# Kernel tuning notes

Hardware: AMD Instinct MI355X
Metric: run time of the kernel (lower is better)

## Reference

```python
import jax, jax.numpy as jnp
import numpy as np

STEPS = 3


def setup_inputs() -> dict:
    key = jax.random.key(0)
    ks = jax.random.split(key, 6)
    N, H, B = 1000000, 128, 16384
    x = jax.random.normal(ks[0], (N, H), dtype=jnp.float32)
    batch_vec = jnp.sort(jax.random.randint(ks[1], (N,), 0, B)).astype(jnp.int64)
    scale_ih = 1.0 / np.sqrt(2 * H)
    scale_hh = 1.0 / np.sqrt(H)
    W_ih = jax.random.normal(ks[2], (4 * H, 2 * H), dtype=jnp.float32) * scale_ih
    W_hh = jax.random.normal(ks[3], (4 * H, H), dtype=jnp.float32) * scale_hh
    b_ih = jnp.zeros((4 * H,), dtype=jnp.float32)
    b_hh = jnp.zeros((4 * H,), dtype=jnp.float32)
    return {"x": x, "batch_vec": batch_vec, "W_ih": W_ih, "W_hh": W_hh,
            "b_ih": b_ih, "b_hh": b_hh, "num_graphs": B}


def _set2set(x, batch_vec, W_ih, W_hh, b_ih, b_hh, B):
    N, H = x.shape
    q_star = jnp.zeros((B, 2 * H), x.dtype)
    h = jnp.zeros((B, H), x.dtype)
    c = jnp.zeros((B, H), x.dtype)
    bias = b_ih + b_hh
    for _ in range(STEPS):
        # LSTMCell (torch gate order: i, f, g, o)
        gates = q_star @ W_ih.T + h @ W_hh.T + bias  # [B, 4H]
        i, f, g, o = jnp.split(gates, 4, axis=-1)
        c = jax.nn.sigmoid(f) * c + jax.nn.sigmoid(i) * jnp.tanh(g)
        h = jax.nn.sigmoid(o) * jnp.tanh(c)
        q = h  # [B, H]
        # attention logits per node
        e = jnp.sum(x * q[batch_vec], axis=-1)  # [N]
        emax = jax.ops.segment_max(e, batch_vec, num_segments=B)
        emax = jax.lax.stop_gradient(jnp.where(jnp.isfinite(emax), emax, 0.0))
        ex = jnp.exp(e - emax[batch_vec])
        denom = jax.ops.segment_sum(ex, batch_vec, num_segments=B)
        a = ex / denom[batch_vec]  # segment softmax, [N]
        r = jax.ops.segment_sum(a[:, None] * x, batch_vec, num_segments=B)  # [B, H]
        q_star = jnp.concatenate([q, r], axis=-1)  # [B, 2H]
    return q_star


def reference(x, batch_vec, W_ih, W_hh, b_ih, b_hh, num_graphs):
    return _set2set(x, batch_vec, W_ih, W_hh, b_ih, b_hh, int(num_graphs))
```

## Files before the change

### kernel.cpp

```cpp
#include <hip/hip_runtime.h>
#include <math.h>

#define HDIM 128
#define G4 512
#define TS 36

typedef float vf4 __attribute__((ext_vector_type(4)));
typedef unsigned short u16x8 __attribute__((ext_vector_type(8)));

__device__ __forceinline__ float sigm(float v) { return 1.0f / (1.0f + __expf(-v)); }
__device__ __forceinline__ float ftanh(float v) {
    return 1.0f - 2.0f / (__expf(2.0f * v) + 1.0f);
}
__device__ __forceinline__ float dot4(vf4 a, vf4 b) {
    return a.x * b.x + a.y * b.y + a.z * b.z + a.w * b.w;
}
__device__ __forceinline__ vf4 ldnt4(const float* p) {
    return __builtin_nontemporal_load((const vf4*)p);
}
__device__ __forceinline__ unsigned short f2bf(float f) {
    unsigned u = __float_as_uint(f);
    u += 0x7fff + ((u >> 16) & 1);
    return (unsigned short)(u >> 16);
}
__device__ __forceinline__ float bf2f(unsigned short h) {
    return __uint_as_float(((unsigned)h) << 16);
}

__global__ __launch_bounds__(256) void k_setup(const float* __restrict__ W_ih,
                                               const float* __restrict__ W_hh,
                                               const float* __restrict__ b_ih,
                                               const float* __restrict__ b_hh,
                                               const int* __restrict__ batch_vec, int N, int B,
                                               float* __restrict__ Wc, int* __restrict__ seg_start,
                                               float* __restrict__ gh0) {
    __shared__ float h0s[HDIM];
    int t = blockIdx.x * 256 + threadIdx.x;
    if (blockIdx.x < 2) {
        if (threadIdx.x < HDIM) {
            int hid = threadIdx.x;
            float bi = b_ih[hid] + b_hh[hid];
            float bg = b_ih[2 * HDIM + hid] + b_hh[2 * HDIM + hid];
            float bo = b_ih[3 * HDIM + hid] + b_hh[3 * HDIM + hid];
            float c0 = sigm(bi) * ftanh(bg);
            h0s[hid] = sigm(bo) * ftanh(c0);
        }
        __syncthreads();
        if (t < G4) {
            float s = 0.0f;
#pragma unroll
            for (int k = 0; k < HDIM; k += 4) {
                vf4 wi = *(const vf4*)(W_ih + (size_t)t * 256 + k);
                vf4 wh = *(const vf4*)(W_hh + (size_t)t * HDIM + k);
                s += (wi.x + wh.x) * h0s[k] + (wi.y + wh.y) * h0s[k + 1] +
                     (wi.z + wh.z) * h0s[k + 2] + (wi.w + wh.w) * h0s[k + 3];
            }
            gh0[t] = s;
        }
    }
    if (t < G4 * 2 * HDIM) {
        int g = t >> 8;
        int k = t & 255;
        float w = W_ih[g * 256 + k];
        if (k < HDIM) w += W_hh[g * HDIM + k];
        Wc[t] = w;
    }
    if (t <= B) {
        int lo = 0, hi = N;
        while (lo < hi) {
            int mid = (lo + hi) >> 1;
            if (batch_vec[mid] < t) lo = mid + 1; else hi = mid;
        }
        seg_start[t] = lo;
    }
}

__global__ __launch_bounds__(256) void k_cvt(const float* __restrict__ x,
                                             unsigned short* __restrict__ x16,
                                             long total8) {
    long i = (long)blockIdx.x * 256 + threadIdx.x;
    long stride = (long)gridDim.x * 256;
    for (; i < total8; i += stride) {
        vf4 a = ldnt4(x + i * 8);
        vf4 b = ldnt4(x + i * 8 + 4);
        u16x8 c;
        c[0] = f2bf(a.x); c[1] = f2bf(a.y); c[2] = f2bf(a.z); c[3] = f2bf(a.w);
        c[4] = f2bf(b.x); c[5] = f2bf(b.y); c[6] = f2bf(b.z); c[7] = f2bf(b.w);
        *(u16x8*)(x16 + i * 8) = c;
    }
}

#define UPD(m_, d_, ra_, rb_, p_, xa_, xb_)  \
    {                                        \
        float mn_ = fmaxf(m_, p_);           \
        float sc_ = __expf(m_ - mn_);        \
        float pe_ = __expf(p_ - mn_);        \
        d_ = d_ * sc_ + pe_;                 \
        ra_ = ra_ * sc_ + pe_ * xa_;         \
        rb_ = rb_ * sc_ + pe_ * xb_;         \
        m_ = mn_;                            \
    }

#define SHFL16(p_)                  \
    p_ += __shfl_xor(p_, 1, 64);    \
    p_ += __shfl_xor(p_, 2, 64);    \
    p_ += __shfl_xor(p_, 4, 64);    \
    p_ += __shfl_xor(p_, 8, 64);

__global__ __launch_bounds__(256) void k_attn(const unsigned short* __restrict__ x16,
                                              const float* __restrict__ q, int ldq,
                                              const float* __restrict__ b_ih,
                                              const float* __restrict__ b_hh,
                                              const int* __restrict__ seg_start,
                                              float* __restrict__ r_out, int ldr, int col_off,
                                              int B) {
    int wave = threadIdx.x >> 6;
    int lane = threadIdx.x & 63;
    int l16 = lane & 15;
    int quarter = lane >> 4;
    int nblk = gridDim.x;
    int bid = blockIdx.x;
    int q8 = nblk >> 3, r8 = nblk & 7;
    int xcd = bid & 7, pos = bid >> 3;
    int nb = (xcd < r8 ? xcd * (q8 + 1) : r8 * (q8 + 1) + (xcd - r8) * q8) + pos;
    int seg = (nb << 2) + wave;
    if (seg >= B) return;
    int s = seg_start[seg], e = seg_start[seg + 1];

    vf4 qa, qb;
    if (q) {
        const float* qrow = q + (size_t)seg * ldq + l16 * 8;
        qa = *(const vf4*)qrow;
        qb = *(const vf4*)(qrow + 4);
    } else {
        int c = l16 * 8;
        vf4 bi0 = *(const vf4*)(b_ih + c) + *(const vf4*)(b_hh + c);
        vf4 bi1 = *(const vf4*)(b_ih + c + 4) + *(const vf4*)(b_hh + c + 4);
        vf4 bg0 = *(const vf4*)(b_ih + 2 * HDIM + c) + *(const vf4*)(b_hh + 2 * HDIM + c);
        vf4 bg1 = *(const vf4*)(b_ih + 2 * HDIM + c + 4) + *(const vf4*)(b_hh + 2 * HDIM + c + 4);
        vf4 bo0 = *(const vf4*)(b_ih + 3 * HDIM + c) + *(const vf4*)(b_hh + 3 * HDIM + c);
        vf4 bo1 = *(const vf4*)(b_ih + 3 * HDIM + c + 4) + *(const vf4*)(b_hh + 3 * HDIM + c + 4);
#pragma unroll
        for (int j = 0; j < 4; ++j) {
            float c0 = sigm(bi0[j]) * ftanh(bg0[j]);
            qa[j] = sigm(bo0[j]) * ftanh(c0);
            float c1 = sigm(bi1[j]) * ftanh(bg1[j]);
            qb[j] = sigm(bo1[j]) * ftanh(c1);
        }
    }

    float m0 = 0.0f, d0 = 0.0f, m1 = 0.0f, d1 = 0.0f;
    vf4 ra0 = {0.f, 0.f, 0.f, 0.f}, rb0 = {0.f, 0.f, 0.f, 0.f};
    vf4 ra1 = {0.f, 0.f, 0.f, 0.f}, rb1 = {0.f, 0.f, 0.f, 0.f};

    int base = s;
#pragma unroll 1
    for (; base + 16 <= e; base += 16) {
        vf4 xa[4], xb[4];
        float p[4];
#pragma unroll
        for (int t = 0; t < 4; ++t) {
            const unsigned short* xr = x16 + (size_t)(base + quarter + 4 * t) * HDIM + l16 * 8;
            u16x8 u = *(const u16x8*)xr;
            xa[t] = vf4{bf2f(u[0]), bf2f(u[1]), bf2f(u[2]), bf2f(u[3])};
            xb[t] = vf4{bf2f(u[4]), bf2f(u[5]), bf2f(u[6]), bf2f(u[7])};
        }
#pragma unroll
        for (int t = 0; t < 4; ++t) p[t] = dot4(xa[t], qa) + dot4(xb[t], qb);
        SHFL16(p[0]) SHFL16(p[1]) SHFL16(p[2]) SHFL16(p[3])
        UPD(m0, d0, ra0, rb0, p[0], xa[0], xb[0])
        UPD(m1, d1, ra1, rb1, p[1], xa[1], xb[1])
        UPD(m0, d0, ra0, rb0, p[2], xa[2], xb[2])
        UPD(m1, d1, ra1, rb1, p[3], xa[3], xb[3])
    }
#pragma unroll 1
    for (; base < e; base += 4) {
        int row = base + quarter;
        const unsigned short* xr = x16 + (size_t)min(row, e - 1) * HDIM + l16 * 8;
        u16x8 u = *(const u16x8*)xr;
        vf4 xa = {bf2f(u[0]), bf2f(u[1]), bf2f(u[2]), bf2f(u[3])};
        vf4 xb = {bf2f(u[4]), bf2f(u[5]), bf2f(u[6]), bf2f(u[7])};
        float p = dot4(xa, qa) + dot4(xb, qb);
        SHFL16(p)
        if (row >= e) p = -1e30f;
        UPD(m0, d0, ra0, rb0, p, xa, xb)
    }
    {
        float M = fmaxf(m0, m1);
        float w0 = __expf(m0 - M), w1 = __expf(m1 - M);
        d0 = d0 * w0 + d1 * w1;
        ra0 = ra0 * w0 + ra1 * w1;
        rb0 = rb0 * w0 + rb1 * w1;
        m0 = M;
    }
#pragma unroll
    for (int off = 16; off <= 32; off <<= 1) {
        float om = __shfl_xor(m0, off, 64);
        float M = fmaxf(m0, om);
        float w = __expf(m0 - M);
        d0 *= w; ra0 *= w; rb0 *= w;
        d0 += __shfl_xor(d0, off, 64);
        ra0.x += __shfl_xor(ra0.x, off, 64);
        ra0.y += __shfl_xor(ra0.y, off, 64);
        ra0.z += __shfl_xor(ra0.z, off, 64);
        ra0.w += __shfl_xor(ra0.w, off, 64);
        rb0.x += __shfl_xor(rb0.x, off, 64);
        rb0.y += __shfl_xor(rb0.y, off, 64);
        rb0.z += __shfl_xor(rb0.z, off, 64);
        rb0.w += __shfl_xor(rb0.w, off, 64);
        m0 = M;
    }
    float inv = (d0 > 0.0f) ? 1.0f / d0 : 0.0f;
    if (quarter == 0) {
        float* dst = r_out + (size_t)seg * ldr + col_off + l16 * 8;
        *(vf4*)dst = ra0 * inv;
        *(vf4*)(dst + 4) = rb0 * inv;
    }
}

__global__ __launch_bounds__(256) void k_gemm_lstm1(const float* __restrict__ r_prev,
                                                    const float* __restrict__ Wc,
                                                    const float* __restrict__ gh0,
                                                    const float* __restrict__ b_ih,
                                                    const float* __restrict__ b_hh,
                                                    float* __restrict__ h_new,
                                                    float* __restrict__ c_new) {
    __shared__ float As[128 * TS];
    __shared__ float Ws[64 * TS];
    int ct = blockIdx.y;
    int rb = blockIdx.x * 128;
    int tid = threadIdx.x;
    int tx = tid & 15, ty = tid >> 4;
    float acc[8][4];
#pragma unroll
    for (int i = 0; i < 8; ++i)
#pragma unroll
        for (int j = 0; j < 4; ++j) acc[i][j] = 0.0f;

    for (int kc = 0; kc < 4; ++kc) {
        int kbase = kc * 32;
#pragma unroll
        for (int i = 0; i < 4; ++i) {
            int li = tid + i * 256;
            int row = li >> 3;
            int c4 = (li & 7) * 4;
            *(vf4*)&As[row * TS + c4] = *(const vf4*)(r_prev + (size_t)(rb + row) * HDIM + kbase + c4);
        }
#pragma unroll
        for (int i = 0; i < 2; ++i) {
            int li = tid + i * 256;
            int col = li >> 3;
            int c4 = (li & 7) * 4;
            int g = ct * 16 + (col & 15) + 128 * (col >> 4);
            *(vf4*)&Ws[col * TS + c4] = *(const vf4*)(Wc + (size_t)g * 256 + 128 + kbase + c4);
        }
        __syncthreads();
#pragma unroll
        for (int k = 0; k < 32; k += 4) {
            vf4 a[8], b[4];
#pragma unroll
            for (int i = 0; i < 8; ++i) a[i] = *(vf4*)&As[(ty + 16 * i) * TS + k];
#pragma unroll
            for (int j = 0; j < 4; ++j) b[j] = *(vf4*)&Ws[(tx + 16 * j) * TS + k];
#pragma unroll
            for (int i = 0; i < 8; ++i)
#pragma unroll
                for (int j = 0; j < 4; ++j) {
                    acc[i][j] += a[i].x * b[j].x + a[i].y * b[j].y +
                                 a[i].z * b[j].z + a[i].w * b[j].w;
                }
        }
        __syncthreads();
    }
    int hidx = ct * 16 + tx;
    float bi = b_ih[hidx] + b_hh[hidx] + gh0[hidx];
    float bf = b_ih[HDIM + hidx] + b_hh[HDIM + hidx] + gh0[HDIM + hidx];
    float bg = b_ih[2 * HDIM + hidx] + b_hh[2 * HDIM + hidx] + gh0[2 * HDIM + hidx];
    float bo = b_ih[3 * HDIM + hidx] + b_hh[3 * HDIM + hidx] + gh0[3 * HDIM + hidx];
    float bi0 = b_ih[hidx] + b_hh[hidx];
    float bg0 = b_ih[2 * HDIM + hidx] + b_hh[2 * HDIM + hidx];
    float c0 = sigm(bi0) * ftanh(bg0);
#pragma unroll
    for (int i = 0; i < 8; ++i) {
        int row = rb + ty + 16 * i;
        float gi = acc[i][0] + bi;
        float gf = acc[i][1] + bf;
        float gg = acc[i][2] + bg;
        float go = acc[i][3] + bo;
        float cn = sigm(gf) * c0 + sigm(gi) * ftanh(gg);
        float hn = sigm(go) * ftanh(cn);
        c_new[(size_t)row * HDIM + hidx] = cn;
        h_new[(size_t)row * HDIM + hidx] = hn;
    }
}

__global__ __launch_bounds__(256) void k_gemm_lstm(const float* __restrict__ h_prev,
                                                   const float* __restrict__ r_prev,
                                                   const float* __restrict__ c_prev,
                                                   const float* __restrict__ Wc,
                                                   const float* __restrict__ b_ih,
                                                   const float* __restrict__ b_hh,
                                                   float* __restrict__ h_mirror) {
    __shared__ float As[128 * TS];
    __shared__ float Ws[64 * TS];
    int ct = blockIdx.y;
    int rb = blockIdx.x * 128;
    int tid = threadIdx.x;
    int tx = tid & 15, ty = tid >> 4;
    float acc[8][4];
#pragma unroll
    for (int i = 0; i < 8; ++i)
#pragma unroll
        for (int j = 0; j < 4; ++j) acc[i][j] = 0.0f;

    for (int kc = 0; kc < 8; ++kc) {
        const float* src = (kc < 4) ? h_prev : r_prev;
        int kbase = (kc & 3) * 32;
#pragma unroll
        for (int i = 0; i < 4; ++i) {
            int li = tid + i * 256;
            int row = li >> 3;
            int c4 = (li & 7) * 4;
            *(vf4*)&As[row * TS + c4] = *(const vf4*)(src + (size_t)(rb + row) * HDIM + kbase + c4);
        }
#pragma unroll
        for (int i = 0; i < 2; ++i) {
            int li = tid + i * 256;
            int col = li >> 3;
            int c4 = (li & 7) * 4;
            int g = ct * 16 + (col & 15) + 128 * (col >> 4);
            *(vf4*)&Ws[col * TS + c4] = *(const vf4*)(Wc + (size_t)g * 256 + kc * 32 + c4);
        }
        __syncthreads();
#pragma unroll
        for (int k = 0; k < 32; k += 4) {
            vf4 a[8], b[4];
#pragma unroll
            for (int i = 0; i < 8; ++i) a[i] = *(vf4*)&As[(ty + 16 * i) * TS + k];
#pragma unroll
            for (int j = 0; j < 4; ++j) b[j] = *(vf4*)&Ws[(tx + 16 * j) * TS + k];
#pragma unroll
            for (int i = 0; i < 8; ++i)
#pragma unroll
                for (int j = 0; j < 4; ++j) {
                    acc[i][j] += a[i].x * b[j].x + a[i].y * b[j].y +
                                 a[i].z * b[j].z + a[i].w * b[j].w;
                }
        }
        __syncthreads();
    }
    int hidx = ct * 16 + tx;
    float bi = b_ih[hidx] + b_hh[hidx];
    float bf = b_ih[HDIM + hidx] + b_hh[HDIM + hidx];
    float bg = b_ih[2 * HDIM + hidx] + b_hh[2 * HDIM + hidx];
    float bo = b_ih[3 * HDIM + hidx] + b_hh[3 * HDIM + hidx];
#pragma unroll
    for (int i = 0; i < 8; ++i) {
        int row = rb + ty + 16 * i;
        float gi = acc[i][0] + bi;
        float gf = acc[i][1] + bf;
        float gg = acc[i][2] + bg;
        float go = acc[i][3] + bo;
        float cp = c_prev[(size_t)row * HDIM + hidx];
        float cn = sigm(gf) * cp + sigm(gi) * ftanh(gg);
        float hn = sigm(go) * ftanh(cn);
        h_mirror[(size_t)row * 2 * HDIM + hidx] = hn;
    }
}

extern "C" void kernel_launch(void* const* d_in, const int* in_sizes, int n_in,
                              void* d_out, int out_size, void* d_ws, size_t ws_size,
                              hipStream_t stream) {
    const float* x = (const float*)d_in[0];
    const int* batch_vec = (const int*)d_in[1];
    const float* W_ih = (const float*)d_in[2];
    const float* W_hh = (const float*)d_in[3];
    const float* b_ih = (const float*)d_in[4];
    const float* b_hh = (const float*)d_in[5];
    float* out = (float*)d_out;

    int N = in_sizes[1];
    int B = out_size / (2 * HDIM);

    char* ws = (char*)d_ws;
    float* Wc = (float*)ws;            ws += (size_t)G4 * 2 * HDIM * 4;
    float* gh0 = (float*)ws;           ws += (size_t)G4 * 4;
    float* h_b = (float*)ws;           ws += (size_t)B * HDIM * 4;
    float* cbuf = (float*)ws;          ws += (size_t)B * HDIM * 4;
    float* rbuf = (float*)ws;          ws += (size_t)B * HDIM * 4;
    int* seg = (int*)ws;               ws += (size_t)(B + 1) * 4;
    ws = (char*)(((size_t)ws + 255) & ~(size_t)255);
    unsigned short* x16 = (unsigned short*)ws;

    k_setup<<<512, 256, 0, stream>>>(W_ih, W_hh, b_ih, b_hh, batch_vec, N, B, Wc, seg, gh0);
    k_cvt<<<2048, 256, 0, stream>>>(x, x16, (long)N * HDIM / 8);

    dim3 ggrid(B / 128, 8);
    int ablk = (B + 3) / 4;
    k_attn<<<ablk, 256, 0, stream>>>(x16, nullptr, 0, b_ih, b_hh, seg, rbuf, HDIM, 0, B);
    k_gemm_lstm1<<<ggrid, 256, 0, stream>>>(rbuf, Wc, gh0, b_ih, b_hh, h_b, cbuf);
    k_attn<<<ablk, 256, 0, stream>>>(x16, h_b, HDIM, b_ih, b_hh, seg, rbuf, HDIM, 0, B);
    k_gemm_lstm<<<ggrid, 256, 0, stream>>>(h_b, rbuf, cbuf, Wc, b_ih, b_hh, out);
    k_attn<<<ablk, 256, 0, stream>>>(x16, out, 2 * HDIM, b_ih, b_hh, seg, out, 2 * HDIM, HDIM, B);
}
```

Baseline: 476.7 us.

## Fuse bf16 conversion into first attention pass and give each 16-lane group one segment

Drops the separate fp32-to-bf16 conversion kernel. The first attention pass now reads fp32 x directly, converts it, and writes x16 while computing the step-0 attention. This removes one full extra read of x. All attention passes now map one segment to each 16-lane quarter instead of one per wave, with software-prefetched rows and no cross-quarter reduction, and the middle pass walks blocks in reverse order to reuse cached x16 data. The risks are load imbalance inside a wave when segment lengths differ, since every quarter loops to the longest segment, plus higher register pressure from the prefetch buffers.

```diff
diff --git a/kernel.cpp b/kernel.cpp
--- a/kernel.cpp
+++ b/kernel.cpp
@@ -75,21 +75,6 @@
     }
 }
 
-__global__ __launch_bounds__(256) void k_cvt(const float* __restrict__ x,
-                                             unsigned short* __restrict__ x16,
-                                             long total8) {
-    long i = (long)blockIdx.x * 256 + threadIdx.x;
-    long stride = (long)gridDim.x * 256;
-    for (; i < total8; i += stride) {
-        vf4 a = ldnt4(x + i * 8);
-        vf4 b = ldnt4(x + i * 8 + 4);
-        u16x8 c;
-        c[0] = f2bf(a.x); c[1] = f2bf(a.y); c[2] = f2bf(a.z); c[3] = f2bf(a.w);
-        c[4] = f2bf(b.x); c[5] = f2bf(b.y); c[6] = f2bf(b.z); c[7] = f2bf(b.w);
-        *(u16x8*)(x16 + i * 8) = c;
-    }
-}
-
 #define UPD(m_, d_, ra_, rb_, p_, xa_, xb_)  \
     {                                        \
         float mn_ = fmaxf(m_, p_);           \
@@ -107,32 +92,68 @@
     p_ += __shfl_xor(p_, 4, 64);    \
     p_ += __shfl_xor(p_, 8, 64);
 
-__global__ __launch_bounds__(256) void k_attn(const unsigned short* __restrict__ x16,
-                                              const float* __restrict__ q, int ldq,
-                                              const float* __restrict__ b_ih,
-                                              const float* __restrict__ b_hh,
-                                              const int* __restrict__ seg_start,
-                                              float* __restrict__ r_out, int ldr, int col_off,
-                                              int B) {
+struct AttState {
+    float m0, d0, m1, d1;
+    vf4 ra0, rb0, ra1, rb1;
+};
+
+__device__ __forceinline__ void init_state(AttState& st) {
+    st.m0 = 0.f; st.d0 = 0.f; st.m1 = 0.f; st.d1 = 0.f;
+    st.ra0 = vf4{0.f, 0.f, 0.f, 0.f}; st.rb0 = vf4{0.f, 0.f, 0.f, 0.f};
+    st.ra1 = vf4{0.f, 0.f, 0.f, 0.f}; st.rb1 = vf4{0.f, 0.f, 0.f, 0.f};
+}
+
+__device__ __forceinline__ void compute4(const vf4 xa[4], const vf4 xb[4], int baserow, int e,
+                                         vf4 qa, vf4 qb, AttState& st) {
+    float p[4];
+#pragma unroll
+    for (int t = 0; t < 4; ++t) p[t] = dot4(xa[t], qa) + dot4(xb[t], qb);
+    SHFL16(p[0]) SHFL16(p[1]) SHFL16(p[2]) SHFL16(p[3])
+#pragma unroll
+    for (int t = 0; t < 4; ++t)
+        if (baserow + t >= e) p[t] = -1e30f;
+    UPD(st.m0, st.d0, st.ra0, st.rb0, p[0], xa[0], xb[0])
+    UPD(st.m1, st.d1, st.ra1, st.rb1, p[1], xa[1], xb[1])
+    UPD(st.m0, st.d0, st.ra0, st.rb0, p[2], xa[2], xb[2])
+    UPD(st.m1, st.d1, st.ra1, st.rb1, p[3], xa[3], xb[3])
+}
+
+__device__ __forceinline__ void finish_state(AttState& st, float* dst) {
+    float M = fmaxf(st.m0, st.m1);
+    float w0 = __expf(st.m0 - M), w1 = __expf(st.m1 - M);
+    float d = st.d0 * w0 + st.d1 * w1;
+    vf4 ra = st.ra0 * w0 + st.ra1 * w1;
+    vf4 rb = st.rb0 * w0 + st.rb1 * w1;
+    float inv = (d > 0.0f) ? 1.0f / d : 0.0f;
+    *(vf4*)dst = ra * inv;
+    *(vf4*)(dst + 4) = rb * inv;
+}
+
+__device__ __forceinline__ int seg_of_block(int bid, int nblk, int rev, int wave, int quarter) {
+    int q8 = nblk >> 3, r8 = nblk & 7;
+    int xcd = bid & 7, pos = bid >> 3;
+    int nb = (xcd < r8 ? xcd * (q8 + 1) : r8 * (q8 + 1) + (xcd - r8) * q8) + pos;
+    if (rev) nb = nblk - 1 - nb;
+    return nb * 16 + wave * 4 + quarter;
+}
+
+__global__ __launch_bounds__(256) void k_attn_cvt(const float* __restrict__ x,
+                                                  unsigned short* __restrict__ x16,
+                                                  const float* __restrict__ b_ih,
+                                                  const float* __restrict__ b_hh,
+                                                  const int* __restrict__ seg_start,
+                                                  float* __restrict__ r_out, int B) {
     int wave = threadIdx.x >> 6;
     int lane = threadIdx.x & 63;
     int l16 = lane & 15;
     int quarter = lane >> 4;
-    int nblk = gridDim.x;
-    int bid = blockIdx.x;
-    int q8 = nblk >> 3, r8 = nblk & 7;
-    int xcd = bid & 7, pos = bid >> 3;
-    int nb = (xcd < r8 ? xcd * (q8 + 1) : r8 * (q8 + 1) + (xcd - r8) * q8) + pos;
-    int seg = (nb << 2) + wave;
-    if (seg >= B) return;
-    int s = seg_start[seg], e = seg_start[seg + 1];
+    int seg = seg_of_block(blockIdx.x, gridDim.x, 0, wave, quarter);
+    int seg_c = min(seg, B - 1);
+    int s = seg_start[seg_c], e = seg_start[seg_c + 1];
+    if (seg >= B) { s = 0; e = 0; }
 
     vf4 qa, qb;
-    if (q) {
-        const float* qrow = q + (size_t)seg * ldq + l16 * 8;
-        qa = *(const vf4*)qrow;
-        qb = *(const vf4*)(qrow + 4);
-    } else {
+    {
         int c = l16 * 8;
         vf4 bi0 = *(const vf4*)(b_ih + c) + *(const vf4*)(b_hh + c);
         vf4 bi1 = *(const vf4*)(b_ih + c + 4) + *(const vf4*)(b_hh + c + 4);
@@ -149,73 +170,124 @@
         }
     }
 
-    float m0 = 0.0f, d0 = 0.0f, m1 = 0.0f, d1 = 0.0f;
-    vf4 ra0 = {0.f, 0.f, 0.f, 0.f}, rb0 = {0.f, 0.f, 0.f, 0.f};
-    vf4 ra1 = {0.f, 0.f, 0.f, 0.f}, rb1 = {0.f, 0.f, 0.f, 0.f};
-
+    int iters = (e - s + 3) >> 2;
+    iters = max(iters, __shfl_xor(iters, 16, 64));
+    iters = max(iters, __shfl_xor(iters, 32, 64));
+    iters = max(iters, 1);
+
+    AttState st;
+    init_state(st);
+
+    vf4 ca[4], cb[4];
+#pragma unroll
+    for (int t = 0; t < 4; ++t) {
+        int rl = max(min(s + t, e - 1), 0);
+        const float* xr = x + (size_t)rl * HDIM + l16 * 8;
+        ca[t] = ldnt4(xr);
+        cb[t] = ldnt4(xr + 4);
+    }
     int base = s;
 #pragma unroll 1
-    for (; base + 16 <= e; base += 16) {
+    for (int j = 1; j < iters; ++j) {
+        vf4 na[4], nb[4];
+#pragma unroll
+        for (int t = 0; t < 4; ++t) {
+            int rl = max(min(s + 4 * j + t, e - 1), 0);
+            const float* xr = x + (size_t)rl * HDIM + l16 * 8;
+            na[t] = ldnt4(xr);
+            nb[t] = ldnt4(xr + 4);
+        }
+#pragma unroll
+        for (int t = 0; t < 4; ++t) {
+            if (base + t < e) {
+                u16x8 cv;
+                cv[0] = f2bf(ca[t].x); cv[1] = f2bf(ca[t].y); cv[2] = f2bf(ca[t].z); cv[3] = f2bf(ca[t].w);
+                cv[4] = f2bf(cb[t].x); cv[5] = f2bf(cb[t].y); cv[6] = f2bf(cb[t].z); cv[7] = f2bf(cb[t].w);
+                *(u16x8*)(x16 + (size_t)(base + t) * HDIM + l16 * 8) = cv;
+            }
+        }
+        compute4(ca, cb, base, e, qa, qb, st);
+#pragma unroll
+        for (int t = 0; t < 4; ++t) { ca[t] = na[t]; cb[t] = nb[t]; }
+        base += 4;
+    }
+#pragma unroll
+    for (int t = 0; t < 4; ++t) {
+        if (base + t < e) {
+            u16x8 cv;
+            cv[0] = f2bf(ca[t].x); cv[1] = f2bf(ca[t].y); cv[2] = f2bf(ca[t].z); cv[3] = f2bf(ca[t].w);
+            cv[4] = f2bf(cb[t].x); cv[5] = f2bf(cb[t].y); cv[6] = f2bf(cb[t].z); cv[7] = f2bf(cb[t].w);
+            *(u16x8*)(x16 + (size_t)(base + t) * HDIM + l16 * 8) = cv;
+        }
+    }
+    compute4(ca, cb, base, e, qa, qb, st);
+
+    if (seg < B) finish_state(st, r_out + (size_t)seg * HDIM + l16 * 8);
+}
+
+__global__ __launch_bounds__(256) void k_attn_b16(const unsigned short* __restrict__ x16,
+                                                  const float* __restrict__ q, int ldq,
+                                                  const int* __restrict__ seg_start,
+                                                  float* __restrict__ r_out, int ldr, int col_off,
+                                                  int B, int rev) {
+    int wave = threadIdx.x >> 6;
+    int lane = threadIdx.x & 63;
+    int l16 = lane & 15;
+    int quarter = lane >> 4;
+    int seg = seg_of_block(blockIdx.x, gridDim.x, rev, wave, quarter);
+    int seg_c = min(seg, B - 1);
+    int s = seg_start[seg_c], e = seg_start[seg_c + 1];
+    if (seg >= B) { s = 0; e = 0; }
+
+    const float* qrow = q + (size_t)seg_c * ldq + l16 * 8;
+    vf4 qa = *(const vf4*)qrow;
+    vf4 qb = *(const vf4*)(qrow + 4);
+
+    int iters = (e - s + 3) >> 2;
+    iters = max(iters, __shfl_xor(iters, 16, 64));
+    iters = max(iters, __shfl_xor(iters, 32, 64));
+    iters = max(iters, 1);
+
+    AttState st;
+    init_state(st);
+
+    u16x8 cur[4];
+#pragma unroll
+    for (int t = 0; t < 4; ++t) {
+        int rl = max(min(s + t, e - 1), 0);
+        cur[t] = *(const u16x8*)(x16 + (size_t)rl * HDIM + l16 * 8);
+    }
+    int base = s;
+#pragma unroll 1
+    for (int j = 1; j < iters; ++j) {
+        u16x8 nxt[4];
+#pragma unroll
+        for (int t = 0; t < 4; ++t) {
+            int rl = max(min(s + 4 * j + t, e - 1), 0);
+            nxt[t] = *(const u16x8*)(x16 + (size_t)rl * HDIM + l16 * 8);
+        }
         vf4 xa[4], xb[4];
-        float p[4];
 #pragma unroll
         for (int t = 0; t < 4; ++t) {
-            const unsigned short* xr = x16 + (size_t)(base + quarter + 4 * t) * HDIM + l16 * 8;
-            u16x8 u = *(const u16x8*)xr;
-            xa[t] = vf4{bf2f(u[0]), bf2f(u[1]), bf2f(u[2]), bf2f(u[3])};
-            xb[t] = vf4{bf2f(u[4]), bf2f(u[5]), bf2f(u[6]), bf2f(u[7])};
-        }
-#pragma unroll
-        for (int t = 0; t < 4; ++t) p[t] = dot4(xa[t], qa) + dot4(xb[t], qb);
-        SHFL16(p[0]) SHFL16(p[1]) SHFL16(p[2]) SHFL16(p[3])
-        UPD(m0, d0, ra0, rb0, p[0], xa[0], xb[0])
-        UPD(m1, d1, ra1, rb1, p[1], xa[1], xb[1])
-        UPD(m0, d0, ra0, rb0, p[2], xa[2], xb[2])
-        UPD(m1, d1, ra1, rb1, p[3], xa[3], xb[3])
-    }
-#pragma unroll 1
-    for (; base < e; base += 4) {
-        int row = base + quarter;
-        const unsigned short* xr = x16 + (size_t)min(row, e - 1) * HDIM + l16 * 8;
-        u16x8 u = *(const u16x8*)xr;
-        vf4 xa = {bf2f(u[0]), bf2f(u[1]), bf2f(u[2]), bf2f(u[3])};
-        vf4 xb = {bf2f(u[4]), bf2f(u[5]), bf2f(u[6]), bf2f(u[7])};
-        float p = dot4(xa, qa) + dot4(xb, qb);
-        SHFL16(p)
-        if (row >= e) p = -1e30f;
-        UPD(m0, d0, ra0, rb0, p, xa, xb)
+            xa[t] = vf4{bf2f(cur[t][0]), bf2f(cur[t][1]), bf2f(cur[t][2]), bf2f(cur[t][3])};
+            xb[t] = vf4{bf2f(cur[t][4]), bf2f(cur[t][5]), bf2f(cur[t][6]), bf2f(cur[t][7])};
+        }
+        compute4(xa, xb, base, e, qa, qb, st);
+#pragma unroll
+        for (int t = 0; t < 4; ++t) cur[t] = nxt[t];
+        base += 4;
     }
     {
-        float M = fmaxf(m0, m1);
-        float w0 = __expf(m0 - M), w1 = __expf(m1 - M);
-        d0 = d0 * w0 + d1 * w1;
-        ra0 = ra0 * w0 + ra1 * w1;
-        rb0 = rb0 * w0 + rb1 * w1;
-        m0 = M;
-    }
-#pragma unroll
-    for (int off = 16; off <= 32; off <<= 1) {
-        float om = __shfl_xor(m0, off, 64);
-        float M = fmaxf(m0, om);
-        float w = __expf(m0 - M);
-        d0 *= w; ra0 *= w; rb0 *= w;
-        d0 += __shfl_xor(d0, off, 64);
-        ra0.x += __shfl_xor(ra0.x, off, 64);
-        ra0.y += __shfl_xor(ra0.y, off, 64);
-        ra0.z += __shfl_xor(ra0.z, off, 64);
-        ra0.w += __shfl_xor(ra0.w, off, 64);
-        rb0.x += __shfl_xor(rb0.x, off, 64);
-        rb0.y += __shfl_xor(rb0.y, off, 64);
-        rb0.z += __shfl_xor(rb0.z, off, 64);
-        rb0.w += __shfl_xor(rb0.w, off, 64);
-        m0 = M;
-    }
-    float inv = (d0 > 0.0f) ? 1.0f / d0 : 0.0f;
-    if (quarter == 0) {
-        float* dst = r_out + (size_t)seg * ldr + col_off + l16 * 8;
-        *(vf4*)dst = ra0 * inv;
-        *(vf4*)(dst + 4) = rb0 * inv;
-    }
+        vf4 xa[4], xb[4];
+#pragma unroll
+        for (int t = 0; t < 4; ++t) {
+            xa[t] = vf4{bf2f(cur[t][0]), bf2f(cur[t][1]), bf2f(cur[t][2]), bf2f(cur[t][3])};
+            xb[t] = vf4{bf2f(cur[t][4]), bf2f(cur[t][5]), bf2f(cur[t][6]), bf2f(cur[t][7])};
+        }
+        compute4(xa, xb, base, e, qa, qb, st);
+    }
+
+    if (seg < B) finish_state(st, r_out + (size_t)seg * ldr + col_off + l16 * 8);
 }
 
 __global__ __launch_bounds__(256) void k_gemm_lstm1(const float* __restrict__ r_prev,
@@ -393,13 +465,12 @@
     unsigned short* x16 = (unsigned short*)ws;
 
     k_setup<<<512, 256, 0, stream>>>(W_ih, W_hh, b_ih, b_hh, batch_vec, N, B, Wc, seg, gh0);
-    k_cvt<<<2048, 256, 0, stream>>>(x, x16, (long)N * HDIM / 8);
 
     dim3 ggrid(B / 128, 8);
-    int ablk = (B + 3) / 4;
-    k_attn<<<ablk, 256, 0, stream>>>(x16, nullptr, 0, b_ih, b_hh, seg, rbuf, HDIM, 0, B);
+    int ablk = (B + 15) / 16;
+    k_attn_cvt<<<ablk, 256, 0, stream>>>(x, x16, b_ih, b_hh, seg, rbuf, B);
     k_gemm_lstm1<<<ggrid, 256, 0, stream>>>(rbuf, Wc, gh0, b_ih, b_hh, h_b, cbuf);
-    k_attn<<<ablk, 256, 0, stream>>>(x16, h_b, HDIM, b_ih, b_hh, seg, rbuf, HDIM, 0, B);
+    k_attn_b16<<<ablk, 256, 0, stream>>>(x16, h_b, HDIM, seg, rbuf, HDIM, 0, B, 1);
     k_gemm_lstm<<<ggrid, 256, 0, stream>>>(h_b, rbuf, cbuf, Wc, b_ih, b_hh, out);
-    k_attn<<<ablk, 256, 0, stream>>>(x16, out, 2 * HDIM, b_ih, b_hh, seg, out, 2 * HDIM, HDIM, B);
-}
+    k_attn_b16<<<ablk, 256, 0, stream>>>(x16, out, 2 * HDIM, seg, out, 2 * HDIM, HDIM, B, 0);
+}
```

New measurement: 456.4 us. 4.2% less time.
